# Kernel optimization log

Measured on AMD Instinct MI355X. Metric: run time of the kernel, lower is better.

The kernel has to match this reference:

```python
import jax, jax.numpy as jnp
import numpy as np

D_MODEL = 1024
NUM_HEADS = 16
D_K = D_MODEL // NUM_HEADS


def setup_inputs() -> dict:
    key = jax.random.key(0)
    k_x, k_q, k_k, k_v, k_o = jax.random.split(key, 5)
    x = jax.random.normal(k_x, (4, 2048, D_MODEL), dtype=jnp.float32)
    s = 1.0 / np.sqrt(D_MODEL)
    W_q = jax.random.normal(k_q, (D_MODEL, D_MODEL), dtype=jnp.float32) * s
    W_k = jax.random.normal(k_k, (D_MODEL, D_MODEL), dtype=jnp.float32) * s
    W_v = jax.random.normal(k_v, (D_MODEL, D_MODEL), dtype=jnp.float32) * s
    W_o = jax.random.normal(k_o, (D_MODEL, D_MODEL), dtype=jnp.float32) * s
    return {"x": x, "W_q": W_q, "W_k": W_k, "W_v": W_v, "W_o": W_o}


def reference(x, W_q, W_k, W_v, W_o):
    B, S, D = x.shape
    H, dk = NUM_HEADS, D_K
    # Linear layers: y = x @ W.T (torch nn.Linear convention)
    Q = (x @ W_q.T).reshape(B, S, H, dk).transpose(0, 2, 1, 3)  # [B,H,S,dk]
    K = (x @ W_k.T).reshape(B, S, H, dk).transpose(0, 2, 1, 3)
    V = (x @ W_v.T).reshape(B, S, H, dk).transpose(0, 2, 1, 3)
    scores = jnp.einsum('bhqd,bhkd->bhqk', Q, K) / np.sqrt(dk)  # [B,H,S,S]
    causal_mask = jnp.tril(jnp.ones((S, S), dtype=bool))
    scores = jnp.where(causal_mask, scores, -jnp.inf)
    weights = jax.nn.softmax(scores, axis=-1)
    attn = jnp.einsum('bhqk,bhkd->bhqd', weights, V)  # [B,H,S,dk]
    attn = attn.transpose(0, 2, 1, 3).reshape(B, S, D)
    return attn @ W_o.T
```

## Files before the change

kernel.cpp:

```cpp
#include <hip/hip_runtime.h>

#define S_LEN 2048
#define DM 1024
#define NH 16
#define DK 64
#define KE 3072
#define DKE 192

typedef _Float16 f16x8 __attribute__((ext_vector_type(8)));
typedef _Float16 f16x4 __attribute__((ext_vector_type(4)));
typedef float f32x4 __attribute__((ext_vector_type(4)));

#if __has_builtin(__builtin_amdgcn_global_load_lds)
#define HAVE_GLDS 1
__device__ __forceinline__ void gload_lds16(const void* g, void* l) {
    __builtin_amdgcn_global_load_lds((const __attribute__((address_space(1))) void*)g,
                                     (__attribute__((address_space(3))) void*)l, 16, 0, 0);
}
#endif

__global__ __launch_bounds__(256) void k_split_x(const float* __restrict__ x,
                                                 _Float16* __restrict__ Xs) {
    int t = blockIdx.x * 256 + threadIdx.x;
    int m = t >> 8, c = t & 255, k = c * 4;
    f32x4 v = *(const f32x4*)(x + (size_t)m * DM + k);
    f16x4 h, l;
    for (int i = 0; i < 4; ++i) { h[i] = (_Float16)v[i]; l[i] = (_Float16)(v[i] - (float)h[i]); }
    _Float16* row = Xs + (size_t)m * KE;
    *(f16x4*)(row + k) = h;
    *(f16x4*)(row + DM + k) = h;
    *(f16x4*)(row + 2 * DM + k) = l;
}

__global__ __launch_bounds__(256) void k_split_w(const float* __restrict__ Wq, const float* __restrict__ Wk,
                                                 const float* __restrict__ Wv, const float* __restrict__ Wo,
                                                 _Float16* __restrict__ WsQKV, _Float16* __restrict__ WsO) {
    int t = blockIdx.x * 256 + threadIdx.x;
    int n = t >> 8, c = t & 255, k = c * 4;
    const float* src; _Float16* dst;
    if (n < 3072) {
        int sel = n >> 10, nr = n & 1023;
        src = (sel == 0 ? Wq : sel == 1 ? Wk : Wv) + (size_t)nr * DM;
        dst = WsQKV + (size_t)n * KE;
    } else {
        src = Wo + (size_t)(n - 3072) * DM;
        dst = WsO + (size_t)(n - 3072) * KE;
    }
    f32x4 v = *(const f32x4*)(src + k);
    f16x4 h, l;
    for (int i = 0; i < 4; ++i) { h[i] = (_Float16)v[i]; l[i] = (_Float16)(v[i] - (float)h[i]); }
    *(f16x4*)(dst + k) = h;
    *(f16x4*)(dst + DM + k) = l;
    *(f16x4*)(dst + 2 * DM + k) = h;
}

__global__ __launch_bounds__(256) void k_gemm(const _Float16* __restrict__ A,
                                              const _Float16* __restrict__ Bm,
                                              float* __restrict__ C, int N) {
    __shared__ _Float16 lA[128 * 32];
    __shared__ _Float16 lB[128 * 32];
    const int tid = threadIdx.x, lane = tid & 63, wave = tid >> 6;
    const int m0 = blockIdx.y * 128, n0 = blockIdx.x * 128;
    const int wm = (wave >> 1) * 64, wn = (wave & 1) * 64;
    const int r = lane & 15, g = lane >> 4;
    f32x4 acc[4][4] = {};
    const int NT = KE / 32;

#ifdef HAVE_GLDS
    for (int kt = 0; kt < NT; ++kt) {
        const int k0 = kt * 32;
        __syncthreads();
        #pragma unroll
        for (int i = 0; i < 2; ++i) {
            const int v = i * 256 + tid;
            const int row = v >> 2, ch = v & 3;
            gload_lds16(A + (size_t)(m0 + row) * KE + k0 + ch * 8, lA + 8 * (size_t)v);
            gload_lds16(Bm + (size_t)(n0 + row) * KE + k0 + ch * 8, lB + 8 * (size_t)v);
        }
        __syncthreads();
        f16x8 af[4], bf[4];
        #pragma unroll
        for (int i = 0; i < 4; ++i) {
            af[i] = *(const f16x8*)(lA + (wm + i * 16 + r) * 32 + g * 8);
            bf[i] = *(const f16x8*)(lB + (wn + i * 16 + r) * 32 + g * 8);
        }
        #pragma unroll
        for (int i = 0; i < 4; ++i)
            #pragma unroll
            for (int j = 0; j < 4; ++j)
                acc[i][j] = __builtin_amdgcn_mfma_f32_16x16x32_f16(af[i], bf[j], acc[i][j], 0, 0, 0);
    }
#else
    f16x8 ra[2], rb[2];
    auto gload = [&](int kt) {
        int k0 = kt * 32;
        for (int i = 0; i < 2; ++i) {
            int v = i * 256 + tid;
            int row = v >> 2, ch = v & 3;
            ra[i] = *(const f16x8*)(A + (size_t)(m0 + row) * KE + k0 + ch * 8);
            rb[i] = *(const f16x8*)(Bm + (size_t)(n0 + row) * KE + k0 + ch * 8);
        }
    };
    gload(0);
    for (int kt = 0; kt < NT; ++kt) {
        __syncthreads();
        for (int i = 0; i < 2; ++i) {
            int v = i * 256 + tid;
            int row = v >> 2, ch = v & 3;
            *(f16x8*)(lA + row * 32 + ch * 8) = ra[i];
            *(f16x8*)(lB + row * 32 + ch * 8) = rb[i];
        }
        gload(kt + 1 < NT ? kt + 1 : kt);
        __syncthreads();
        f16x8 af[4], bf[4];
        for (int i = 0; i < 4; ++i) {
            af[i] = *(const f16x8*)(lA + (wm + i * 16 + r) * 32 + g * 8);
            bf[i] = *(const f16x8*)(lB + (wn + i * 16 + r) * 32 + g * 8);
        }
        for (int i = 0; i < 4; ++i)
            for (int j = 0; j < 4; ++j)
                acc[i][j] = __builtin_amdgcn_mfma_f32_16x16x32_f16(af[i], bf[j], acc[i][j], 0, 0, 0);
    }
#endif
    for (int i = 0; i < 4; ++i)
        for (int j = 0; j < 4; ++j)
            for (int rr = 0; rr < 4; ++rr) {
                int row = m0 + wm + i * 16 + g * 4 + rr;
                int col = n0 + wn + j * 16 + r;
                C[(size_t)row * N + col] = acc[i][j][rr];
            }
}

__global__ __launch_bounds__(256) void k_reformat_qk(const float* __restrict__ QKV,
                                                     _Float16* __restrict__ Qexp,
                                                     _Float16* __restrict__ Kexp) {
    int t = blockIdx.x * 256 + threadIdx.x;
    int part = t >> 21;
    int u = t & 2097151;
    int m = u >> 8, c = u & 255, k = c * 4;
    f32x4 v = *(const f32x4*)(QKV + (size_t)m * KE + part * DM + k);
    if (part == 0) for (int i = 0; i < 4; ++i) v[i] *= 0.125f;
    f16x4 h, l;
    for (int i = 0; i < 4; ++i) { h[i] = (_Float16)v[i]; l[i] = (_Float16)(v[i] - (float)h[i]); }
    int b = m >> 11, s = m & 2047;
    int hh = k >> 6, d = k & 63;
    _Float16* rowp = (part ? Kexp : Qexp) + ((size_t)(b * NH + hh) * S_LEN + s) * DKE;
    if (part == 0) {
        *(f16x4*)(rowp + d) = h;
        *(f16x4*)(rowp + DK + d) = h;
        *(f16x4*)(rowp + 2 * DK + d) = l;
    } else {
        *(f16x4*)(rowp + d) = h;
        *(f16x4*)(rowp + DK + d) = l;
        *(f16x4*)(rowp + 2 * DK + d) = h;
    }
}

__global__ __launch_bounds__(256) void k_transpose_v(const float* __restrict__ QKV,
                                                     _Float16* __restrict__ Vth,
                                                     _Float16* __restrict__ Vtl) {
    __shared__ float tile[64][65];
    const int bh = blockIdx.y, s0 = blockIdx.x * 64;
    const int tid = threadIdx.x, tx = tid & 63, ty = tid >> 6;
    const int b = bh >> 4, h = bh & 15;
    for (int i = 0; i < 16; ++i) {
        int sl = ty + i * 4;
        tile[sl][tx] = QKV[((size_t)b * S_LEN + s0 + sl) * KE + 2 * DM + h * DK + tx];
    }
    __syncthreads();
    for (int i = 0; i < 16; ++i) {
        int d = ty + i * 4;
        float v = tile[tx][d];
        _Float16 hh = (_Float16)v;
        size_t off = ((size_t)bh * DK + d) * S_LEN + s0 + tx;
        Vth[off] = hh;
        Vtl[off] = (_Float16)(v - (float)hh);
    }
}

__global__ __launch_bounds__(256) void k_flash(const _Float16* __restrict__ Qexp,
                                               const _Float16* __restrict__ Kexp,
                                               const _Float16* __restrict__ Vth,
                                               const _Float16* __restrict__ Vtl,
                                               _Float16* __restrict__ Aexp) {
    __shared__ _Float16 kt_lds[32][200];
    __shared__ _Float16 vh_lds[64][40];
    __shared__ _Float16 vl_lds[64][40];
    __shared__ float p_lds[4][16][36];

    const int bh = blockIdx.y, pair = blockIdx.x;
    const int tid = threadIdx.x, lane = tid & 63, wave = tid >> 6;
    const int r = lane & 15, g = lane >> 4;
    const int b = bh >> 4, h = bh & 15;
    const float LOG2E = 1.44269504088896f;
    const float PC = -3.31233645f;

    const int krow0 = tid / 24,        kc0 = tid % 24;
    const int krow1 = (256 + tid) / 24, kc1 = (256 + tid) % 24;
    const int krow2 = (512 + tid) / 24, kc2 = (512 + tid) % 24;
    const int vrow = tid >> 2, vc = tid & 3;

    f16x8 kpre0, kpre1, kpre2, vhp, vlp;
    auto prefetch = [&](int k0) {
        const _Float16* kb = Kexp + ((size_t)bh * S_LEN + k0) * DKE;
        kpre0 = *(const f16x8*)(kb + (size_t)krow0 * DKE + kc0 * 8);
        kpre1 = *(const f16x8*)(kb + (size_t)krow1 * DKE + kc1 * 8);
        kpre2 = *(const f16x8*)(kb + (size_t)krow2 * DKE + kc2 * 8);
        size_t vo = ((size_t)bh * DK + vrow) * S_LEN + k0 + vc * 8;
        vhp = *(const f16x8*)(Vth + vo);
        vlp = *(const f16x8*)(Vtl + vo);
    };
    auto stage_write = [&]() {
        *(f16x8*)(&kt_lds[krow0][kc0 * 8]) = kpre0;
        *(f16x8*)(&kt_lds[krow1][kc1 * 8]) = kpre1;
        *(f16x8*)(&kt_lds[krow2][kc2 * 8]) = kpre2;
        *(f16x8*)(&vh_lds[vrow][vc * 8]) = vhp;
        *(f16x8*)(&vl_lds[vrow][vc * 8]) = vlp;
    };

    prefetch(0);

    for (int half = 0; half < 2; ++half) {
        const int qt = half ? pair : (31 - pair);
        const int q0 = qt * 64;
        const int qw = q0 + wave * 16;

        f16x8 qf[6];
        {
            const _Float16* qp = Qexp + ((size_t)bh * S_LEN + qw + r) * DKE;
            #pragma unroll
            for (int j = 0; j < 6; ++j) qf[j] = *(const f16x8*)(qp + j * 32 + g * 8);
        }
        f32x4 o[4] = {};
        float l_acc[4] = {0.f, 0.f, 0.f, 0.f};

        const int nkv = 2 * qt + 2;
        for (int kt = 0; kt < nkv; ++kt) {
            int k0 = kt * 32;
            __syncthreads();
            stage_write();
            prefetch(kt + 1 < nkv ? k0 + 32 : 0);
            __syncthreads();

            if (k0 <= qw + 15) {
                f32x4 sc[2] = {};
                #pragma unroll
                for (int nf = 0; nf < 2; ++nf)
                    #pragma unroll
                    for (int j = 0; j < 6; ++j) {
                        f16x8 kf = *(const f16x8*)(&kt_lds[nf * 16 + r][j * 32 + g * 8]);
                        sc[nf] = __builtin_amdgcn_mfma_f32_16x16x32_f16(qf[j], kf, sc[nf], 0, 0, 0);
                    }
                #pragma unroll
                for (int nf = 0; nf < 2; ++nf)
                    #pragma unroll
                    for (int rr = 0; rr < 4; ++rr) {
                        int key = k0 + nf * 16 + r;
                        int q = qw + g * 4 + rr;
                        if (key > q) sc[nf][rr] = -1e30f;
                    }
                f32x4 p[2];
                #pragma unroll
                for (int nf = 0; nf < 2; ++nf)
                    #pragma unroll
                    for (int j = 0; j < 4; ++j) p[nf][j] = exp2f(sc[nf][j] * LOG2E + PC);
                #pragma unroll
                for (int j = 0; j < 4; ++j) l_acc[j] += p[0][j] + p[1][j];
                #pragma unroll
                for (int nf = 0; nf < 2; ++nf)
                    #pragma unroll
                    for (int j = 0; j < 4; ++j)
                        p_lds[wave][g * 4 + j][nf * 16 + r] = p[nf][j];
                f16x8 ph, pl;
                {
                    const float* pr = &p_lds[wave][r][g * 8];
                    f32x4 p0 = *(const f32x4*)(pr);
                    f32x4 p1 = *(const f32x4*)(pr + 4);
                    #pragma unroll
                    for (int jj = 0; jj < 4; ++jj) {
                        _Float16 h0 = (_Float16)p0[jj]; ph[jj] = h0; pl[jj] = (_Float16)(p0[jj] - (float)h0);
                        _Float16 h1 = (_Float16)p1[jj]; ph[4 + jj] = h1; pl[4 + jj] = (_Float16)(p1[jj] - (float)h1);
                    }
                }
                #pragma unroll
                for (int df = 0; df < 4; ++df) {
                    f16x8 vh = *(const f16x8*)(&vh_lds[df * 16 + r][g * 8]);
                    f16x8 vl = *(const f16x8*)(&vl_lds[df * 16 + r][g * 8]);
                    o[df] = __builtin_amdgcn_mfma_f32_16x16x32_f16(ph, vh, o[df], 0, 0, 0);
                    o[df] = __builtin_amdgcn_mfma_f32_16x16x32_f16(ph, vl, o[df], 0, 0, 0);
                    o[df] = __builtin_amdgcn_mfma_f32_16x16x32_f16(pl, vh, o[df], 0, 0, 0);
                }
            }
        }
        float lt[4];
        #pragma unroll
        for (int j = 0; j < 4; ++j) lt[j] = l_acc[j];
        for (int d = 1; d < 16; d <<= 1)
            #pragma unroll
            for (int j = 0; j < 4; ++j) lt[j] += __shfl_xor(lt[j], d);
        #pragma unroll
        for (int j = 0; j < 4; ++j) {
            float inv = 1.0f / lt[j];
            size_t mrow = (size_t)b * S_LEN + qw + g * 4 + j;
            _Float16* orow = Aexp + mrow * KE;
            #pragma unroll
            for (int df = 0; df < 4; ++df) {
                float val = o[df][j] * inv;
                _Float16 hh = (_Float16)val;
                _Float16 ll = (_Float16)(val - (float)hh);
                int col = h * DK + df * 16 + r;
                orow[col] = hh;
                orow[DM + col] = hh;
                orow[2 * DM + col] = ll;
            }
        }
    }
}

extern "C" void kernel_launch(void* const* d_in, const int* in_sizes, int n_in,
                              void* d_out, int out_size, void* d_ws, size_t ws_size,
                              hipStream_t stream) {
    const float* x  = (const float*)d_in[0];
    const float* Wq = (const float*)d_in[1];
    const float* Wk = (const float*)d_in[2];
    const float* Wv = (const float*)d_in[3];
    const float* Wo = (const float*)d_in[4];
    char* ws = (char*)d_ws;
    _Float16* Xs    = (_Float16*)(ws + 0);
    _Float16* WsQKV = (_Float16*)(ws + 50331648);
    _Float16* WsO   = (_Float16*)(ws + 69206016);
    float*    QKV   = (float*)   (ws + 75497472);
    _Float16* Aexp  = (_Float16*)(ws + 75497472);
    _Float16* Qexp  = (_Float16*)(ws + 0);
    _Float16* Kexp  = (_Float16*)(ws + 176160768);
    _Float16* Vth   = (_Float16*)(ws + 226492416);
    _Float16* Vtl   = (_Float16*)(ws + 243269632);

    k_split_x<<<8192, 256, 0, stream>>>(x, Xs);
    k_split_w<<<4096, 256, 0, stream>>>(Wq, Wk, Wv, Wo, WsQKV, WsO);
    k_gemm<<<dim3(24, 64), 256, 0, stream>>>(Xs, WsQKV, QKV, 3072);
    k_reformat_qk<<<16384, 256, 0, stream>>>(QKV, Qexp, Kexp);
    k_transpose_v<<<dim3(32, 64), 256, 0, stream>>>(QKV, Vth, Vtl);
    k_flash<<<dim3(16, 64), 256, 0, stream>>>(Qexp, Kexp, Vth, Vtl, Aexp);
    k_gemm<<<dim3(8, 64), 256, 0, stream>>>(Aexp, WsO, (float*)d_out, 1024);
}
```

Baseline: 625.4 us.

## Fuse Q/K/V reformatting into QKV GEMM epilogue and transpose V in fp16

The QKV projection GEMM now writes scaled, hi/lo-split fp16 Q and K directly in the expanded attention layout, and V as separate hi/lo fp16 planes. This drops the fp32 QKV buffer and the separate reformat kernel. The V transpose then reads fp16 instead of fp32. This removes a large intermediate write and read plus one launch, at the cost of scalar, less coalesced 2-byte stores in the GEMM epilogue and a two-pass transpose.

```diff
diff --git a/kernel.cpp b/kernel.cpp
--- a/kernel.cpp
+++ b/kernel.cpp
@@ -54,9 +54,14 @@
     *(f16x4*)(dst + 2 * DM + k) = h;
 }
 
-__global__ __launch_bounds__(256) void k_gemm(const _Float16* __restrict__ A,
-                                              const _Float16* __restrict__ Bm,
-                                              float* __restrict__ C, int N) {
+template <int MODE>
+__global__ __launch_bounds__(256) void k_gemm_t(const _Float16* __restrict__ A,
+                                                const _Float16* __restrict__ Bm,
+                                                float* __restrict__ C, int N,
+                                                _Float16* __restrict__ Qexp,
+                                                _Float16* __restrict__ Kexp,
+                                                _Float16* __restrict__ Vh,
+                                                _Float16* __restrict__ Vl) {
     __shared__ _Float16 lA[128 * 32];
     __shared__ _Float16 lB[128 * 32];
     const int tid = threadIdx.x, lane = tid & 63, wave = tid >> 6;
@@ -122,59 +127,61 @@
                 acc[i][j] = __builtin_amdgcn_mfma_f32_16x16x32_f16(af[i], bf[j], acc[i][j], 0, 0, 0);
     }
 #endif
+    #pragma unroll
     for (int i = 0; i < 4; ++i)
+        #pragma unroll
         for (int j = 0; j < 4; ++j)
+            #pragma unroll
             for (int rr = 0; rr < 4; ++rr) {
-                int row = m0 + wm + i * 16 + g * 4 + rr;
-                int col = n0 + wn + j * 16 + r;
-                C[(size_t)row * N + col] = acc[i][j][rr];
+                const int row = m0 + wm + i * 16 + g * 4 + rr;
+                const int col = n0 + wn + j * 16 + r;
+                float val = acc[i][j][rr];
+                if constexpr (MODE == 0) {
+                    C[(size_t)row * N + col] = val;
+                } else {
+                    const int part = col >> 10, pc = col & 1023;
+                    const int b = row >> 11, s = row & 2047;
+                    if (part == 2) {
+                        _Float16 hv = (_Float16)val;
+                        Vh[(size_t)row * DM + pc] = hv;
+                        Vl[(size_t)row * DM + pc] = (_Float16)(val - (float)hv);
+                    } else {
+                        const int hh = pc >> 6, d = pc & 63;
+                        _Float16* rowp = (part ? Kexp : Qexp) +
+                                         ((size_t)((b << 4) + hh) * S_LEN + s) * DKE;
+                        if (part == 0) val *= 0.125f;
+                        _Float16 hv = (_Float16)val;
+                        _Float16 lv = (_Float16)(val - (float)hv);
+                        rowp[d] = hv;
+                        rowp[DK + d]     = (part == 0) ? hv : lv;
+                        rowp[2 * DK + d] = (part == 0) ? lv : hv;
+                    }
+                }
             }
 }
 
-__global__ __launch_bounds__(256) void k_reformat_qk(const float* __restrict__ QKV,
-                                                     _Float16* __restrict__ Qexp,
-                                                     _Float16* __restrict__ Kexp) {
-    int t = blockIdx.x * 256 + threadIdx.x;
-    int part = t >> 21;
-    int u = t & 2097151;
-    int m = u >> 8, c = u & 255, k = c * 4;
-    f32x4 v = *(const f32x4*)(QKV + (size_t)m * KE + part * DM + k);
-    if (part == 0) for (int i = 0; i < 4; ++i) v[i] *= 0.125f;
-    f16x4 h, l;
-    for (int i = 0; i < 4; ++i) { h[i] = (_Float16)v[i]; l[i] = (_Float16)(v[i] - (float)h[i]); }
-    int b = m >> 11, s = m & 2047;
-    int hh = k >> 6, d = k & 63;
-    _Float16* rowp = (part ? Kexp : Qexp) + ((size_t)(b * NH + hh) * S_LEN + s) * DKE;
-    if (part == 0) {
-        *(f16x4*)(rowp + d) = h;
-        *(f16x4*)(rowp + DK + d) = h;
-        *(f16x4*)(rowp + 2 * DK + d) = l;
-    } else {
-        *(f16x4*)(rowp + d) = h;
-        *(f16x4*)(rowp + DK + d) = l;
-        *(f16x4*)(rowp + 2 * DK + d) = h;
-    }
-}
-
-__global__ __launch_bounds__(256) void k_transpose_v(const float* __restrict__ QKV,
-                                                     _Float16* __restrict__ Vth,
-                                                     _Float16* __restrict__ Vtl) {
-    __shared__ float tile[64][65];
+__global__ __launch_bounds__(256) void k_transpose_v16(const _Float16* __restrict__ Vh,
+                                                       const _Float16* __restrict__ Vl,
+                                                       _Float16* __restrict__ Vth,
+                                                       _Float16* __restrict__ Vtl) {
+    __shared__ _Float16 tile[64][74];
     const int bh = blockIdx.y, s0 = blockIdx.x * 64;
     const int tid = threadIdx.x, tx = tid & 63, ty = tid >> 6;
     const int b = bh >> 4, h = bh & 15;
-    for (int i = 0; i < 16; ++i) {
-        int sl = ty + i * 4;
-        tile[sl][tx] = QKV[((size_t)b * S_LEN + s0 + sl) * KE + 2 * DM + h * DK + tx];
-    }
-    __syncthreads();
-    for (int i = 0; i < 16; ++i) {
-        int d = ty + i * 4;
-        float v = tile[tx][d];
-        _Float16 hh = (_Float16)v;
-        size_t off = ((size_t)bh * DK + d) * S_LEN + s0 + tx;
-        Vth[off] = hh;
-        Vtl[off] = (_Float16)(v - (float)hh);
+    const _Float16* src = Vh;
+    _Float16* dst = Vth;
+    #pragma unroll
+    for (int pass = 0; pass < 2; ++pass) {
+        if (pass) { src = Vl; dst = Vtl; __syncthreads(); }
+        for (int i = 0; i < 16; ++i) {
+            int sl = ty + i * 4;
+            tile[sl][tx] = src[((size_t)b * S_LEN + s0 + sl) * DM + h * DK + tx];
+        }
+        __syncthreads();
+        for (int i = 0; i < 16; ++i) {
+            int d = ty + i * 4;
+            dst[((size_t)bh * DK + d) * S_LEN + s0 + tx] = tile[tx][d];
+        }
     }
 }
 
@@ -327,20 +334,22 @@
     const float* Wo = (const float*)d_in[4];
     char* ws = (char*)d_ws;
     _Float16* Xs    = (_Float16*)(ws + 0);
+    _Float16* Aexp  = (_Float16*)(ws + 0);
     _Float16* WsQKV = (_Float16*)(ws + 50331648);
     _Float16* WsO   = (_Float16*)(ws + 69206016);
-    float*    QKV   = (float*)   (ws + 75497472);
-    _Float16* Aexp  = (_Float16*)(ws + 75497472);
-    _Float16* Qexp  = (_Float16*)(ws + 0);
-    _Float16* Kexp  = (_Float16*)(ws + 176160768);
-    _Float16* Vth   = (_Float16*)(ws + 226492416);
-    _Float16* Vtl   = (_Float16*)(ws + 243269632);
+    _Float16* Qexp  = (_Float16*)(ws + 75497472);
+    _Float16* Kexp  = (_Float16*)(ws + 125829120);
+    _Float16* Vh    = (_Float16*)(ws + 176160768);
+    _Float16* Vl    = (_Float16*)(ws + 192937984);
+    _Float16* Vth   = (_Float16*)(ws + 209715200);
+    _Float16* Vtl   = (_Float16*)(ws + 226492416);
 
     k_split_x<<<8192, 256, 0, stream>>>(x, Xs);
     k_split_w<<<4096, 256, 0, stream>>>(Wq, Wk, Wv, Wo, WsQKV, WsO);
-    k_gemm<<<dim3(24, 64), 256, 0, stream>>>(Xs, WsQKV, QKV, 3072);
-    k_reformat_qk<<<16384, 256, 0, stream>>>(QKV, Qexp, Kexp);
-    k_transpose_v<<<dim3(32, 64), 256, 0, stream>>>(QKV, Vth, Vtl);
+    k_gemm_t<1><<<dim3(24, 64), 256, 0, stream>>>(Xs, WsQKV, nullptr, 3072,
+                                                  Qexp, Kexp, Vh, Vl);
+    k_transpose_v16<<<dim3(32, 64), 256, 0, stream>>>(Vh, Vl, Vth, Vtl);
     k_flash<<<dim3(16, 64), 256, 0, stream>>>(Qexp, Kexp, Vth, Vtl, Aexp);
-    k_gemm<<<dim3(8, 64), 256, 0, stream>>>(Aexp, WsO, (float*)d_out, 1024);
-}
+    k_gemm_t<0><<<dim3(8, 64), 256, 0, stream>>>(Aexp, WsO, (float*)d_out, 1024,
+                                                 nullptr, nullptr, nullptr, nullptr);
+}
```

Result: faster. 574.7 us (-8.1%).
